# Optimization experiments

Hardware: AMD Instinct MI355X
Metric: run time of the kernel (lower is better)

Reference implementation:

```python
import jax, jax.numpy as jnp
import numpy as np

NUM_CLASSES = 200
MARGIN = 0.6
LAMBDA_WEIGHT = 0.2
ALPHA = 1.5
GAMMA = 0.8
EPS = 1e-8


def setup_inputs() -> dict:
    key = jax.random.key(0)
    k1, k2 = jax.random.split(key)
    B, D = 32768, 512
    features = jax.random.normal(k1, (B, D), dtype=jnp.float32)
    labels = jax.random.randint(k2, (B,), 0, NUM_CLASSES, dtype=jnp.int64)
    return {"features": features, "labels": labels}


def reference(features, labels):
    B, D = features.shape
    C = NUM_CLASSES
    labels = labels.astype(jnp.int32)

    # Per-class prototypes (segment mean), matching mask-sum / (count + eps)
    proto_sum = jax.ops.segment_sum(features, labels, num_segments=C)      # [C, D]
    counts = jax.ops.segment_sum(jnp.ones((B,), features.dtype), labels, num_segments=C)
    prototypes = proto_sum / (counts[:, None] + EPS)                       # [C, D]

    # Squared distances from every sample to every prototype via Gram trick
    f2 = jnp.sum(features * features, axis=1, keepdims=True)               # [B, 1]
    p2 = jnp.sum(prototypes * prototypes, axis=1)                          # [C]
    d2 = jnp.maximum(f2 + p2[None, :] - 2.0 * features @ prototypes.T, 0.0)  # [B, C]

    # Nearest negative prototype: mask out the positive class with +inf
    pos_mask = jnp.arange(C)[None, :] == labels[:, None]                   # [B, C]
    neg_idx = jnp.argmin(jnp.where(pos_mask, jnp.inf, d2), axis=1)         # [B]

    # Exact squared distances to positive / chosen negative prototypes
    pos_proto = prototypes[labels]                                         # [B, D]
    neg_proto = prototypes[neg_idx]                                        # [B, D]
    d_ap = jnp.sum((features - pos_proto) ** 2, axis=1)                    # [B]
    d_an = jnp.sum((features - neg_proto) ** 2, axis=1)                    # [B]

    # Replicate the original's sequential normalization (d_ap is updated first)
    d_ap_n = d_ap / (d_ap + d_an + EPS)
    d_an_n = d_an / (d_ap_n + d_an + EPS)

    per_sample = jnp.maximum(0.0, ALPHA * d_ap_n - GAMMA * d_an_n + MARGIN)
    contrastive_loss = jnp.mean(per_sample)
    return jnp.abs(LAMBDA_WEIGHT * contrastive_loss)
```

## Files before the change

### kernel.cpp

```cpp
#include <hip/hip_runtime.h>
#include <hip/hip_bf16.h>

#define NCLS 200
#define NPAD 208
#define NT 13
#define DIM 512
#define NSAMP 32768
#define CAP 48
#define BM 64
#define BK 32
#define KIT 16
#define BSTR 40

typedef __attribute__((ext_vector_type(4))) float f32x4;
typedef __attribute__((ext_vector_type(4))) int   i32x4;
typedef __attribute__((ext_vector_type(8))) short bf16x8;

__device__ inline short bf16s(float x) {
  __hip_bfloat16 h = __float2bfloat16(x);
  return *reinterpret_cast<short*>(&h);
}

__device__ inline bf16x8 pack8(f32x4 a, f32x4 b) {
  bf16x8 r;
  r[0] = bf16s(a[0]); r[1] = bf16s(a[1]); r[2] = bf16s(a[2]); r[3] = bf16s(a[3]);
  r[4] = bf16s(b[0]); r[5] = bf16s(b[1]); r[6] = bf16s(b[2]); r[7] = bf16s(b[3]);
  return r;
}

__device__ inline float sumsq(f32x4 a) {
  return a[0]*a[0] + a[1]*a[1] + a[2]*a[2] + a[3]*a[3];
}

__global__ __launch_bounds__(512) void k_psum(
    const float* __restrict__ feat, const int* __restrict__ labels,
    float* __restrict__ psum, int* __restrict__ pcnt)
{
  const int bx = blockIdx.x;
  const int c = bx >> 2, q = bx & 3;
  const int tid = threadIdx.x;
  const int lane = tid & 63;
  const int w = tid >> 6;

  __shared__ int   lists[8][CAP];
  __shared__ int   cnts[8];
  __shared__ float partial[8][DIM];

  int cnt = 0;
  const int segbase = q * (NSAMP / 4) + w * (NSAMP / 32);
  for (int i = 0; i < (NSAMP / 32) / 256; ++i) {
    const int base = segbase + i * 256 + lane * 4;
    const i32x4 lab4 = *(const i32x4*)(labels + base);
    #pragma unroll
    for (int u = 0; u < 4; ++u) {
      const bool m = (lab4[u] == c);
      const unsigned long long bal = __ballot(m);
      if (m) {
        const int pos = cnt + __popcll(bal & ((1ull << lane) - 1ull));
        if (pos < CAP) lists[w][pos] = base + u;
      }
      cnt += __popcll(bal);
    }
  }
  if (cnt > CAP) cnt = CAP;
  if (lane == 0) cnts[w] = cnt;

  float acc[8];
  #pragma unroll
  for (int qq = 0; qq < 8; ++qq) acc[qq] = 0.f;
  for (int j = 0; j < cnt; ++j) {
    const int r = lists[w][j];
    const f32x4 a = *(const f32x4*)(feat + (size_t)r * DIM + lane * 8);
    const f32x4 b = *(const f32x4*)(feat + (size_t)r * DIM + lane * 8 + 4);
    acc[0] += a[0]; acc[1] += a[1]; acc[2] += a[2]; acc[3] += a[3];
    acc[4] += b[0]; acc[5] += b[1]; acc[6] += b[2]; acc[7] += b[3];
  }
  #pragma unroll
  for (int qq = 0; qq < 8; ++qq) partial[w][lane * 8 + qq] = acc[qq];
  __syncthreads();

  int total = 0;
  #pragma unroll
  for (int u = 0; u < 8; ++u) total += cnts[u];
  float s = 0.f;
  #pragma unroll
  for (int u = 0; u < 8; ++u) s += partial[u][tid];
  psum[(size_t)(q * NCLS + c) * DIM + tid] = s;
  if (tid == 0) pcnt[q * NCLS + c] = total;
}

__global__ __launch_bounds__(256) void k_pcomb(
    const float* __restrict__ psum, const int* __restrict__ pcnt,
    unsigned short* __restrict__ protoB, float* __restrict__ p2out)
{
  const int c = blockIdx.x;
  const int tid = threadIdx.x;
  if (c >= NCLS) {
    protoB[c * DIM + tid] = 0;
    protoB[c * DIM + 256 + tid] = 0;
    if (tid == 0) p2out[c] = 1e30f;
    return;
  }
  __shared__ float red[256];
  float a0 = 0.f, a1 = 0.f;
  int total = 0;
  #pragma unroll
  for (int q = 0; q < 4; ++q) {
    a0 += psum[(size_t)(q * NCLS + c) * DIM + tid];
    a1 += psum[(size_t)(q * NCLS + c) * DIM + 256 + tid];
    total += pcnt[q * NCLS + c];
  }
  const float inv = 1.0f / ((float)total + 1e-8f);
  const float p0 = a0 * inv, p1 = a1 * inv;
  protoB[c * DIM + tid] = (unsigned short)bf16s(p0);
  protoB[c * DIM + 256 + tid] = (unsigned short)bf16s(p1);

  red[tid] = p0 * p0 + p1 * p1;
  __syncthreads();
  for (int s = 128; s > 0; s >>= 1) {
    if (tid < s) red[tid] += red[tid + s];
    __syncthreads();
  }
  if (tid == 0) p2out[c] = red[0];
}

__global__ __launch_bounds__(256) void k_score(
    const float* __restrict__ feat, const int* __restrict__ labels,
    const unsigned short* __restrict__ protoB, const float* __restrict__ p2,
    float* __restrict__ partials)
{
  __shared__ __align__(16) unsigned short As[2][BM * BK];
  __shared__ __align__(16) unsigned short Bs[2][NPAD * BSTR];
  __shared__ float f2s[BM][4];

  const int tid = threadIdx.x;
  const int lane = tid & 63;
  const int w = tid >> 6;
  const int lr = lane & 15;
  const int kg = lane >> 4;

  const int blockRow = blockIdx.x * BM;

  const int arow = tid >> 2;
  const int apart = tid & 3;
  const float* agp = feat + (size_t)(blockRow + arow) * DIM + apart * 8;
  const int aunit = ((apart ^ (arow & 3)) * 8);
  const int brow = tid;
  const f32x4* bgp = (const f32x4*)(protoB + (size_t)brow * DIM);

  float f2part = 0.f;

  {
    const f32x4 a0 = *(const f32x4*)(agp);
    const f32x4 a1 = *(const f32x4*)(agp + 4);
    f2part += sumsq(a0) + sumsq(a1);
    *(bf16x8*)&As[0][arow * BK + aunit] = pack8(a0, a1);
    if (brow < NPAD) {
      const f32x4 b0 = bgp[0], b1 = bgp[1], b2 = bgp[2], b3 = bgp[3];
      *(f32x4*)&Bs[0][brow * BSTR + 0]  = b0;
      *(f32x4*)&Bs[0][brow * BSTR + 8]  = b1;
      *(f32x4*)&Bs[0][brow * BSTR + 16] = b2;
      *(f32x4*)&Bs[0][brow * BSTR + 24] = b3;
    }
  }
  __syncthreads();

  f32x4 acc[NT];
  #pragma unroll
  for (int n = 0; n < NT; ++n) acc[n] = f32x4{0.f, 0.f, 0.f, 0.f};

  const int r0 = w * 16 + lr;
  const int ar0 = r0 * BK + ((kg ^ (r0 & 3)) * 8);

  #pragma unroll 2
  for (int t = 0; t < KIT; ++t) {
    const int cur = t & 1;
    f32x4 a0, a1, b0, b1, b2, b3;
    if (t < KIT - 1) {
      const float* ag = agp + (t + 1) * BK;
      a0 = *(const f32x4*)(ag);
      a1 = *(const f32x4*)(ag + 4);
      if (brow < NPAD) {
        const f32x4* bg = bgp + (t + 1) * 4;
        b0 = bg[0]; b1 = bg[1]; b2 = bg[2]; b3 = bg[3];
      }
    }
    const bf16x8 Af = *(const bf16x8*)&As[cur][ar0];
    #pragma unroll
    for (int n = 0; n < NT; ++n) {
      const bf16x8 Bf = *(const bf16x8*)&Bs[cur][(n * 16 + lr) * BSTR + kg * 8];
      acc[n] = __builtin_amdgcn_mfma_f32_16x16x32_bf16(Af, Bf, acc[n], 0, 0, 0);
    }
    if (t < KIT - 1) {
      const int nb = cur ^ 1;
      f2part += sumsq(a0) + sumsq(a1);
      *(bf16x8*)&As[nb][arow * BK + aunit] = pack8(a0, a1);
      if (brow < NPAD) {
        *(f32x4*)&Bs[nb][brow * BSTR + 0]  = b0;
        *(f32x4*)&Bs[nb][brow * BSTR + 8]  = b1;
        *(f32x4*)&Bs[nb][brow * BSTR + 16] = b2;
        *(f32x4*)&Bs[nb][brow * BSTR + 24] = b3;
      }
      __syncthreads();
    }
  }

  f2s[arow][apart] = f2part;
  __syncthreads();

  float p2v[NT];
  #pragma unroll
  for (int n = 0; n < NT; ++n) p2v[n] = p2[n * 16 + lr];

  float lsum = 0.f;
  #pragma unroll
  for (int r = 0; r < 4; ++r) {
    const int srow = kg * 4 + r;
    const int lrow = w * 16 + srow;
    const float f2v = (f2s[lrow][0] + f2s[lrow][1]) + (f2s[lrow][2] + f2s[lrow][3]);
    const int samp = blockRow + lrow;
    const int lab = labels[samp];
    float bestd = 1e38f; int bestc = 1 << 30;
    float posd = -1.f;
    #pragma unroll
    for (int n = 0; n < NT; ++n) {
      const int cidx = n * 16 + lr;
      const float sc = acc[n][r];
      const float d2 = fmaxf(f2v + p2v[n] - 2.0f * sc, 0.0f);
      if (cidx == lab) posd = d2;
      else if (cidx < NCLS &&
               (d2 < bestd || (d2 == bestd && cidx < bestc))) { bestd = d2; bestc = cidx; }
    }
    #pragma unroll
    for (int sft = 1; sft < 16; sft <<= 1) {
      const float od = __shfl_xor(bestd, sft);
      const int   oc = __shfl_xor(bestc, sft);
      const float op = __shfl_xor(posd, sft);
      if (od < bestd || (od == bestd && oc < bestc)) { bestd = od; bestc = oc; }
      posd = fmaxf(posd, op);
    }
    const float dap = posd, dan = bestd;
    const float dapn = dap / (dap + dan + 1e-8f);
    const float dann = dan / (dapn + dan + 1e-8f);
    const float ps = fmaxf(0.f, 1.5f * dapn - 0.8f * dann + 0.6f);
    if (lr == 0) lsum += ps;
  }
  lsum += __shfl_xor(lsum, 16);
  lsum += __shfl_xor(lsum, 32);
  if (lane == 0) partials[blockIdx.x * 4 + w] = lsum;
}

__global__ __launch_bounds__(256) void k_finish(const float* __restrict__ partials,
                                                float* __restrict__ out)
{
  __shared__ float red[256];
  const int tid = threadIdx.x;
  float s = 0.f;
  #pragma unroll
  for (int j = 0; j < 8; ++j) s += partials[tid + j * 256];
  red[tid] = s;
  __syncthreads();
  for (int st = 128; st > 0; st >>= 1) {
    if (tid < st) red[tid] += red[tid + st];
    __syncthreads();
  }
  if (tid == 0) out[0] = fabsf(0.2f * (red[0] / (float)NSAMP));
}

extern "C" void kernel_launch(void* const* d_in, const int* in_sizes, int n_in,
                              void* d_out, int out_size, void* d_ws, size_t ws_size,
                              hipStream_t stream) {
  const float* feat = (const float*)d_in[0];
  const int* labels = (const int*)d_in[1];
  float* out = (float*)d_out;

  char* ws = (char*)d_ws;
  unsigned short* protoB = (unsigned short*)ws;
  float* p2 = (float*)(ws + 212992);
  float* partials = (float*)(ws + 214016);
  float* psum = (float*)(ws + 229376);
  int* pcnt = (int*)(ws + 229376 + 1638400);

  k_psum<<<4 * NCLS, 512, 0, stream>>>(feat, labels, psum, pcnt);
  k_pcomb<<<NPAD, 256, 0, stream>>>(psum, pcnt, protoB, p2);
  k_score<<<512, 256, 0, stream>>>(feat, labels, protoB, p2, partials);
  k_finish<<<1, 256, 0, stream>>>(partials, out);
}
```

Measured before the change: 50.22 us.

## Restructure prototype and score kernels with 2x2 wave tiling and k-major prototype layout

Splits the prototype summation across 8 sample segments per class instead of 4 and unrolls the row accumulation with two accumulator sets. Prototypes are stored k-major in 32-wide tiles so each K-step's B tile load is contiguous. The score kernel now uses a 2x2 wave layout where each wave covers 32 rows by 112 columns, reusing each B fragment across two A fragments, and merges the argmin across column halves through shared memory. Explicit double-buffer register prefetch with lighter barriers and a 2-blocks-per-CU launch bound are added. The costs are more psum traffic, padding to 224 classes, and extra shared-memory reduction work.

```diff
diff --git a/kernel.cpp b/kernel.cpp
--- a/kernel.cpp
+++ b/kernel.cpp
@@ -2,11 +2,12 @@
 #include <hip/hip_bf16.h>
 
 #define NCLS 200
-#define NPAD 208
-#define NT 13
+#define NPADP 224
+#define NTW 7
 #define DIM 512
 #define NSAMP 32768
-#define CAP 48
+#define NSEG 8
+#define CAP 32
 #define BM 64
 #define BK 32
 #define KIT 16
@@ -32,12 +33,17 @@
   return a[0]*a[0] + a[1]*a[1] + a[2]*a[2] + a[3]*a[3];
 }
 
+__device__ inline void bar_lgkm() {
+  asm volatile("s_waitcnt lgkmcnt(0)" ::: "memory");
+  __builtin_amdgcn_s_barrier();
+}
+
 __global__ __launch_bounds__(512) void k_psum(
     const float* __restrict__ feat, const int* __restrict__ labels,
     float* __restrict__ psum, int* __restrict__ pcnt)
 {
   const int bx = blockIdx.x;
-  const int c = bx >> 2, q = bx & 3;
+  const int c = bx >> 3, s = bx & 7;
   const int tid = threadIdx.x;
   const int lane = tid & 63;
   const int w = tid >> 6;
@@ -47,8 +53,9 @@
   __shared__ float partial[8][DIM];
 
   int cnt = 0;
-  const int segbase = q * (NSAMP / 4) + w * (NSAMP / 32);
-  for (int i = 0; i < (NSAMP / 32) / 256; ++i) {
+  const int segbase = s * (NSAMP / NSEG) + w * (NSAMP / NSEG / 8);
+  #pragma unroll
+  for (int i = 0; i < 2; ++i) {
     const int base = segbase + i * 256 + lane * 4;
     const i32x4 lab4 = *(const i32x4*)(labels + base);
     #pragma unroll
@@ -65,39 +72,52 @@
   if (cnt > CAP) cnt = CAP;
   if (lane == 0) cnts[w] = cnt;
 
-  float acc[8];
-  #pragma unroll
-  for (int qq = 0; qq < 8; ++qq) acc[qq] = 0.f;
-  for (int j = 0; j < cnt; ++j) {
-    const int r = lists[w][j];
-    const f32x4 a = *(const f32x4*)(feat + (size_t)r * DIM + lane * 8);
-    const f32x4 b = *(const f32x4*)(feat + (size_t)r * DIM + lane * 8 + 4);
-    acc[0] += a[0]; acc[1] += a[1]; acc[2] += a[2]; acc[3] += a[3];
-    acc[4] += b[0]; acc[5] += b[1]; acc[6] += b[2]; acc[7] += b[3];
-  }
-  #pragma unroll
-  for (int qq = 0; qq < 8; ++qq) partial[w][lane * 8 + qq] = acc[qq];
+  float aE[8], aO[8];
+  #pragma unroll
+  for (int q = 0; q < 8; ++q) { aE[q] = 0.f; aO[q] = 0.f; }
+  int j = 0;
+  for (; j + 2 <= cnt; j += 2) {
+    const int r0 = lists[w][j], r1 = lists[w][j + 1];
+    const f32x4 a0 = *(const f32x4*)(feat + (size_t)r0 * DIM + lane * 8);
+    const f32x4 b0 = *(const f32x4*)(feat + (size_t)r0 * DIM + lane * 8 + 4);
+    const f32x4 a1 = *(const f32x4*)(feat + (size_t)r1 * DIM + lane * 8);
+    const f32x4 b1 = *(const f32x4*)(feat + (size_t)r1 * DIM + lane * 8 + 4);
+    aE[0] += a0[0]; aE[1] += a0[1]; aE[2] += a0[2]; aE[3] += a0[3];
+    aE[4] += b0[0]; aE[5] += b0[1]; aE[6] += b0[2]; aE[7] += b0[3];
+    aO[0] += a1[0]; aO[1] += a1[1]; aO[2] += a1[2]; aO[3] += a1[3];
+    aO[4] += b1[0]; aO[5] += b1[1]; aO[6] += b1[2]; aO[7] += b1[3];
+  }
+  if (j < cnt) {
+    const int r0 = lists[w][j];
+    const f32x4 a0 = *(const f32x4*)(feat + (size_t)r0 * DIM + lane * 8);
+    const f32x4 b0 = *(const f32x4*)(feat + (size_t)r0 * DIM + lane * 8 + 4);
+    aE[0] += a0[0]; aE[1] += a0[1]; aE[2] += a0[2]; aE[3] += a0[3];
+    aE[4] += b0[0]; aE[5] += b0[1]; aE[6] += b0[2]; aE[7] += b0[3];
+  }
+  #pragma unroll
+  for (int q = 0; q < 8; ++q) partial[w][lane * 8 + q] = aE[q] + aO[q];
   __syncthreads();
 
   int total = 0;
   #pragma unroll
   for (int u = 0; u < 8; ++u) total += cnts[u];
-  float s = 0.f;
-  #pragma unroll
-  for (int u = 0; u < 8; ++u) s += partial[u][tid];
-  psum[(size_t)(q * NCLS + c) * DIM + tid] = s;
-  if (tid == 0) pcnt[q * NCLS + c] = total;
+  float sv = 0.f;
+  #pragma unroll
+  for (int u = 0; u < 8; ++u) sv += partial[u][tid];
+  psum[(size_t)(s * NCLS + c) * DIM + tid] = sv;
+  if (tid == 0) pcnt[s * NCLS + c] = total;
 }
 
 __global__ __launch_bounds__(256) void k_pcomb(
     const float* __restrict__ psum, const int* __restrict__ pcnt,
-    unsigned short* __restrict__ protoB, float* __restrict__ p2out)
+    unsigned short* __restrict__ protoI, float* __restrict__ p2out)
 {
   const int c = blockIdx.x;
   const int tid = threadIdx.x;
+  const int d0 = tid, d1 = tid + 256;
   if (c >= NCLS) {
-    protoB[c * DIM + tid] = 0;
-    protoB[c * DIM + 256 + tid] = 0;
+    protoI[((size_t)(d0 >> 5) * NPADP + c) * 32 + (d0 & 31)] = 0;
+    protoI[((size_t)(d1 >> 5) * NPADP + c) * 32 + (d1 & 31)] = 0;
     if (tid == 0) p2out[c] = 1e30f;
     return;
   }
@@ -105,149 +125,179 @@
   float a0 = 0.f, a1 = 0.f;
   int total = 0;
   #pragma unroll
-  for (int q = 0; q < 4; ++q) {
-    a0 += psum[(size_t)(q * NCLS + c) * DIM + tid];
-    a1 += psum[(size_t)(q * NCLS + c) * DIM + 256 + tid];
-    total += pcnt[q * NCLS + c];
+  for (int s = 0; s < NSEG; ++s) {
+    a0 += psum[(size_t)(s * NCLS + c) * DIM + d0];
+    a1 += psum[(size_t)(s * NCLS + c) * DIM + d1];
+    total += pcnt[s * NCLS + c];
   }
   const float inv = 1.0f / ((float)total + 1e-8f);
   const float p0 = a0 * inv, p1 = a1 * inv;
-  protoB[c * DIM + tid] = (unsigned short)bf16s(p0);
-  protoB[c * DIM + 256 + tid] = (unsigned short)bf16s(p1);
+  protoI[((size_t)(d0 >> 5) * NPADP + c) * 32 + (d0 & 31)] = (unsigned short)bf16s(p0);
+  protoI[((size_t)(d1 >> 5) * NPADP + c) * 32 + (d1 & 31)] = (unsigned short)bf16s(p1);
 
   red[tid] = p0 * p0 + p1 * p1;
   __syncthreads();
-  for (int s = 128; s > 0; s >>= 1) {
-    if (tid < s) red[tid] += red[tid + s];
+  for (int st = 128; st > 0; st >>= 1) {
+    if (tid < st) red[tid] += red[tid + st];
     __syncthreads();
   }
   if (tid == 0) p2out[c] = red[0];
 }
 
-__global__ __launch_bounds__(256) void k_score(
+__global__ __launch_bounds__(256, 2) void k_score(
     const float* __restrict__ feat, const int* __restrict__ labels,
-    const unsigned short* __restrict__ protoB, const float* __restrict__ p2,
+    const unsigned short* __restrict__ protoI, const float* __restrict__ p2,
     float* __restrict__ partials)
 {
   __shared__ __align__(16) unsigned short As[2][BM * BK];
-  __shared__ __align__(16) unsigned short Bs[2][NPAD * BSTR];
+  __shared__ __align__(16) unsigned short Bs[2][NPADP * BSTR];
   __shared__ float f2s[BM][4];
+  __shared__ float rd_d[2][BM];
+  __shared__ int   rd_c[2][BM];
+  __shared__ float rd_p[2][BM];
 
   const int tid = threadIdx.x;
   const int lane = tid & 63;
   const int w = tid >> 6;
+  const int wm = w >> 1, wn = w & 1;
   const int lr = lane & 15;
   const int kg = lane >> 4;
-
   const int blockRow = blockIdx.x * BM;
 
-  const int arow = tid >> 2;
-  const int apart = tid & 3;
+  const int arow = tid >> 2, apart = tid & 3;
   const float* agp = feat + (size_t)(blockRow + arow) * DIM + apart * 8;
-  const int aunit = ((apart ^ (arow & 3)) * 8);
+  const int aoff = arow * BK + ((apart ^ (arow & 3)) * 8);
   const int brow = tid;
-  const f32x4* bgp = (const f32x4*)(protoB + (size_t)brow * DIM);
+
+#define ISSUE(T, A0, A1, B0, B1, B2, B3) do {                                   \
+    const float* ag_ = agp + (T) * BK;                                          \
+    A0 = *(const f32x4*)(ag_);                                                  \
+    A1 = *(const f32x4*)(ag_ + 4);                                              \
+    if (brow < NPADP) {                                                         \
+      const f32x4* bg_ = (const f32x4*)(protoI + ((size_t)(T) * NPADP + brow) * 32); \
+      B0 = bg_[0]; B1 = bg_[1]; B2 = bg_[2]; B3 = bg_[3];                       \
+    }                                                                           \
+  } while (0)
+
+#define STORE(NB, A0, A1, B0, B1, B2, B3) do {                                  \
+    f2part += sumsq(A0) + sumsq(A1);                                            \
+    *(bf16x8*)&As[NB][aoff] = pack8(A0, A1);                                    \
+    if (brow < NPADP) {                                                         \
+      *(f32x4*)&Bs[NB][brow * BSTR + 0]  = B0;                                  \
+      *(f32x4*)&Bs[NB][brow * BSTR + 8]  = B1;                                  \
+      *(f32x4*)&Bs[NB][brow * BSTR + 16] = B2;                                  \
+      *(f32x4*)&Bs[NB][brow * BSTR + 24] = B3;                                  \
+    }                                                                           \
+  } while (0)
+
+#define COMPUTE(CUR) do {                                                       \
+    const bf16x8 Af0 = *(const bf16x8*)&As[CUR][ar0];                           \
+    const bf16x8 Af1 = *(const bf16x8*)&As[CUR][ar1];                           \
+    _Pragma("unroll")                                                           \
+    for (int n = 0; n < NTW; ++n) {                                             \
+      const bf16x8 Bf = *(const bf16x8*)&Bs[CUR][boff + n * (16 * BSTR)];       \
+      acc0[n] = __builtin_amdgcn_mfma_f32_16x16x32_bf16(Af0, Bf, acc0[n], 0, 0, 0); \
+      acc1[n] = __builtin_amdgcn_mfma_f32_16x16x32_bf16(Af1, Bf, acc1[n], 0, 0, 0); \
+    }                                                                           \
+  } while (0)
 
   float f2part = 0.f;
-
-  {
-    const f32x4 a0 = *(const f32x4*)(agp);
-    const f32x4 a1 = *(const f32x4*)(agp + 4);
-    f2part += sumsq(a0) + sumsq(a1);
-    *(bf16x8*)&As[0][arow * BK + aunit] = pack8(a0, a1);
-    if (brow < NPAD) {
-      const f32x4 b0 = bgp[0], b1 = bgp[1], b2 = bgp[2], b3 = bgp[3];
-      *(f32x4*)&Bs[0][brow * BSTR + 0]  = b0;
-      *(f32x4*)&Bs[0][brow * BSTR + 8]  = b1;
-      *(f32x4*)&Bs[0][brow * BSTR + 16] = b2;
-      *(f32x4*)&Bs[0][brow * BSTR + 24] = b3;
+  f32x4 aA0, aA1, bA0, bA1, bA2, bA3;
+  f32x4 aB0, aB1, bB0, bB1, bB2, bB3;
+
+  ISSUE(0, aA0, aA1, bA0, bA1, bA2, bA3);
+  STORE(0, aA0, aA1, bA0, bA1, bA2, bA3);
+  ISSUE(1, aB0, aB1, bB0, bB1, bB2, bB3);
+  bar_lgkm();
+
+  f32x4 acc0[NTW], acc1[NTW];
+  #pragma unroll
+  for (int n = 0; n < NTW; ++n) {
+    acc0[n] = f32x4{0.f, 0.f, 0.f, 0.f};
+    acc1[n] = f32x4{0.f, 0.f, 0.f, 0.f};
+  }
+
+  const int r0v = wm * 32 + lr;
+  const int r1v = r0v + 16;
+  const int ar0 = r0v * BK + ((kg ^ (r0v & 3)) * 8);
+  const int ar1 = r1v * BK + ((kg ^ (r1v & 3)) * 8);
+  const int boff = (wn * (NTW * 16) + lr) * BSTR + kg * 8;
+
+  #pragma unroll
+  for (int p = 0; p < KIT / 2; ++p) {
+    const int t0 = 2 * p, t1 = 2 * p + 1;
+    COMPUTE(0);
+    if (t0 + 2 < KIT) ISSUE(t0 + 2, aA0, aA1, bA0, bA1, bA2, bA3);
+    STORE(1, aB0, aB1, bB0, bB1, bB2, bB3);
+    bar_lgkm();
+    COMPUTE(1);
+    if (t1 + 2 < KIT) {
+      ISSUE(t1 + 2, aB0, aB1, bB0, bB1, bB2, bB3);
+      STORE(0, aA0, aA1, bA0, bA1, bA2, bA3);
+      bar_lgkm();
     }
   }
-  __syncthreads();
-
-  f32x4 acc[NT];
-  #pragma unroll
-  for (int n = 0; n < NT; ++n) acc[n] = f32x4{0.f, 0.f, 0.f, 0.f};
-
-  const int r0 = w * 16 + lr;
-  const int ar0 = r0 * BK + ((kg ^ (r0 & 3)) * 8);
-
-  #pragma unroll 2
-  for (int t = 0; t < KIT; ++t) {
-    const int cur = t & 1;
-    f32x4 a0, a1, b0, b1, b2, b3;
-    if (t < KIT - 1) {
-      const float* ag = agp + (t + 1) * BK;
-      a0 = *(const f32x4*)(ag);
-      a1 = *(const f32x4*)(ag + 4);
-      if (brow < NPAD) {
-        const f32x4* bg = bgp + (t + 1) * 4;
-        b0 = bg[0]; b1 = bg[1]; b2 = bg[2]; b3 = bg[3];
+
+  f2s[arow][apart] = f2part;
+  __syncthreads();
+
+  float p2v[NTW];
+  #pragma unroll
+  for (int n = 0; n < NTW; ++n) p2v[n] = p2[wn * (NTW * 16) + n * 16 + lr];
+
+  #pragma unroll
+  for (int m = 0; m < 2; ++m) {
+    #pragma unroll
+    for (int r = 0; r < 4; ++r) {
+      const int srow = kg * 4 + r;
+      const int lrow = wm * 32 + m * 16 + srow;
+      const float f2v = (f2s[lrow][0] + f2s[lrow][1]) + (f2s[lrow][2] + f2s[lrow][3]);
+      const int lab = labels[blockRow + lrow];
+      float bestd = 1e38f; int bestc = 1 << 30;
+      float posd = -1.f;
+      #pragma unroll
+      for (int n = 0; n < NTW; ++n) {
+        const int cidx = wn * (NTW * 16) + n * 16 + lr;
+        const float sc = (m == 0) ? acc0[n][r] : acc1[n][r];
+        const float d2 = fmaxf(f2v + p2v[n] - 2.0f * sc, 0.0f);
+        if (cidx == lab) posd = d2;
+        else if (cidx < NCLS &&
+                 (d2 < bestd || (d2 == bestd && cidx < bestc))) { bestd = d2; bestc = cidx; }
+      }
+      #pragma unroll
+      for (int sft = 1; sft < 16; sft <<= 1) {
+        const float od = __shfl_xor(bestd, sft);
+        const int   oc = __shfl_xor(bestc, sft);
+        const float op = __shfl_xor(posd, sft);
+        if (od < bestd || (od == bestd && oc < bestc)) { bestd = od; bestc = oc; }
+        posd = fmaxf(posd, op);
+      }
+      if (lr == 0) {
+        rd_d[wn][lrow] = bestd; rd_c[wn][lrow] = bestc; rd_p[wn][lrow] = posd;
       }
     }
-    const bf16x8 Af = *(const bf16x8*)&As[cur][ar0];
-    #pragma unroll
-    for (int n = 0; n < NT; ++n) {
-      const bf16x8 Bf = *(const bf16x8*)&Bs[cur][(n * 16 + lr) * BSTR + kg * 8];
-      acc[n] = __builtin_amdgcn_mfma_f32_16x16x32_bf16(Af, Bf, acc[n], 0, 0, 0);
-    }
-    if (t < KIT - 1) {
-      const int nb = cur ^ 1;
-      f2part += sumsq(a0) + sumsq(a1);
-      *(bf16x8*)&As[nb][arow * BK + aunit] = pack8(a0, a1);
-      if (brow < NPAD) {
-        *(f32x4*)&Bs[nb][brow * BSTR + 0]  = b0;
-        *(f32x4*)&Bs[nb][brow * BSTR + 8]  = b1;
-        *(f32x4*)&Bs[nb][brow * BSTR + 16] = b2;
-        *(f32x4*)&Bs[nb][brow * BSTR + 24] = b3;
-      }
-      __syncthreads();
-    }
-  }
-
-  f2s[arow][apart] = f2part;
-  __syncthreads();
-
-  float p2v[NT];
-  #pragma unroll
-  for (int n = 0; n < NT; ++n) p2v[n] = p2[n * 16 + lr];
-
-  float lsum = 0.f;
-  #pragma unroll
-  for (int r = 0; r < 4; ++r) {
-    const int srow = kg * 4 + r;
-    const int lrow = w * 16 + srow;
-    const float f2v = (f2s[lrow][0] + f2s[lrow][1]) + (f2s[lrow][2] + f2s[lrow][3]);
-    const int samp = blockRow + lrow;
-    const int lab = labels[samp];
-    float bestd = 1e38f; int bestc = 1 << 30;
-    float posd = -1.f;
-    #pragma unroll
-    for (int n = 0; n < NT; ++n) {
-      const int cidx = n * 16 + lr;
-      const float sc = acc[n][r];
-      const float d2 = fmaxf(f2v + p2v[n] - 2.0f * sc, 0.0f);
-      if (cidx == lab) posd = d2;
-      else if (cidx < NCLS &&
-               (d2 < bestd || (d2 == bestd && cidx < bestc))) { bestd = d2; bestc = cidx; }
-    }
-    #pragma unroll
-    for (int sft = 1; sft < 16; sft <<= 1) {
-      const float od = __shfl_xor(bestd, sft);
-      const int   oc = __shfl_xor(bestc, sft);
-      const float op = __shfl_xor(posd, sft);
-      if (od < bestd || (od == bestd && oc < bestc)) { bestd = od; bestc = oc; }
-      posd = fmaxf(posd, op);
-    }
+  }
+  __syncthreads();
+
+  if (tid < BM) {
+    const float d0 = rd_d[0][tid], d1 = rd_d[1][tid];
+    const int   c0 = rd_c[0][tid], c1 = rd_c[1][tid];
+    float bestd; int bestc;
+    if (d1 < d0 || (d1 == d0 && c1 < c0)) { bestd = d1; bestc = c1; }
+    else                                  { bestd = d0; bestc = c0; }
+    (void)bestc;
+    const float posd = fmaxf(rd_p[0][tid], rd_p[1][tid]);
     const float dap = posd, dan = bestd;
     const float dapn = dap / (dap + dan + 1e-8f);
     const float dann = dan / (dapn + dan + 1e-8f);
-    const float ps = fmaxf(0.f, 1.5f * dapn - 0.8f * dann + 0.6f);
-    if (lr == 0) lsum += ps;
-  }
-  lsum += __shfl_xor(lsum, 16);
-  lsum += __shfl_xor(lsum, 32);
-  if (lane == 0) partials[blockIdx.x * 4 + w] = lsum;
+    float v = fmaxf(0.f, 1.5f * dapn - 0.8f * dann + 0.6f);
+    #pragma unroll
+    for (int sft = 1; sft < 64; sft <<= 1) v += __shfl_xor(v, sft);
+    if (tid == 0) partials[blockIdx.x] = v;
+  }
+#undef ISSUE
+#undef STORE
+#undef COMPUTE
 }
 
 __global__ __launch_bounds__(256) void k_finish(const float* __restrict__ partials,
@@ -255,10 +305,7 @@
 {
   __shared__ float red[256];
   const int tid = threadIdx.x;
-  float s = 0.f;
-  #pragma unroll
-  for (int j = 0; j < 8; ++j) s += partials[tid + j * 256];
-  red[tid] = s;
+  red[tid] = partials[tid] + partials[tid + 256];
   __syncthreads();
   for (int st = 128; st > 0; st >>= 1) {
     if (tid < st) red[tid] += red[tid + st];
@@ -275,14 +322,14 @@
   float* out = (float*)d_out;
 
   char* ws = (char*)d_ws;
-  unsigned short* protoB = (unsigned short*)ws;
-  float* p2 = (float*)(ws + 212992);
-  float* partials = (float*)(ws + 214016);
-  float* psum = (float*)(ws + 229376);
-  int* pcnt = (int*)(ws + 229376 + 1638400);
-
-  k_psum<<<4 * NCLS, 512, 0, stream>>>(feat, labels, psum, pcnt);
-  k_pcomb<<<NPAD, 256, 0, stream>>>(psum, pcnt, protoB, p2);
-  k_score<<<512, 256, 0, stream>>>(feat, labels, protoB, p2, partials);
+  unsigned short* protoI = (unsigned short*)ws;
+  float* p2 = (float*)(ws + 229376);
+  float* partials = (float*)(ws + 230400);
+  float* psum = (float*)(ws + 232448);
+  int* pcnt = (int*)(ws + 3509248);
+
+  k_psum<<<NSEG * NCLS, 512, 0, stream>>>(feat, labels, psum, pcnt);
+  k_pcomb<<<NPADP, 256, 0, stream>>>(psum, pcnt, protoI, p2);
+  k_score<<<512, 256, 0, stream>>>(feat, labels, protoI, p2, partials);
   k_finish<<<1, 256, 0, stream>>>(partials, out);
 }
```

New measurement: 46.63 us. 1.08x faster.
